# Kernel tuning notes

Measured on AMD Instinct MI355X. Metric: run time of the kernel, lower is better.

The kernel has to match this reference:

```python
import jax, jax.numpy as jnp
import numpy as np

WIN = 9  # window_size (isotropic, module default)
EPS = 1e-5


def _box_sum3d(x, win):
    """Sum over a win^3 box, same-size output ('same' padding). x: [B,1,D,H,W].
    The ones kernel is separable, so apply three 1D convolutions."""
    pad = win // 2
    for ax in range(3):  # spatial axes D,H,W
        kshape = [1, 1, 1, 1, 1]
        kshape[2 + ax] = win
        k = jnp.ones(kshape, x.dtype)
        padding = [(0, 0)] * 3
        padding[ax] = (pad, pad)
        x = jax.lax.conv_general_dilated(x, k, window_strides=(1, 1, 1), padding=padding)
    return x


def setup_inputs() -> dict:
    key = jax.random.key(0)
    k1, k2 = jax.random.split(key)
    shape = (2, 1, 160, 192, 160)
    y_pred = jax.random.normal(k1, shape, dtype=jnp.float32)
    y_true = jax.random.normal(k2, shape, dtype=jnp.float32)
    return {"y_pred": y_pred, "y_true": y_true}


def reference(y_pred, y_true):
    I, J = y_true, y_pred
    win_size = jnp.asarray(WIN ** 3, I.dtype)  # 729

    I_sum = _box_sum3d(I, WIN)
    J_sum = _box_sum3d(J, WIN)
    I2_sum = _box_sum3d(I * I, WIN)
    J2_sum = _box_sum3d(J * J, WIN)
    IJ_sum = _box_sum3d(I * J, WIN)

    I_mean = I_sum / win_size
    J_mean = J_sum / win_size

    cross = IJ_sum - J_mean * I_sum - I_mean * J_sum + I_mean * J_mean * win_size
    I_var = I2_sum - 2 * I_mean * I_sum + I_mean * I_mean * win_size
    J_var = J2_sum - 2 * J_mean * J_sum + J_mean * J_mean * win_size

    cc = cross * cross / (I_var * J_var + EPS)
    return -jnp.mean(cc)
```

## Files before the change

kernel.cpp:

```cpp
#include <hip/hip_runtime.h>
#include <hip/hip_fp16.h>


#define B_    2
#define D_    160
#define H_    192
#define W_    160
#define HW_   (H_*W_)

#define RS    12
#define SLS   (24*RS)
#define FS    (2*SLS)
#define ZROW  (5*FS)
#define ZEND  (ZROW + 16)
#define HSUM0 ZEND
#define HCS   160
#define HRS   10
#define REDU  (HSUM0 + 10*HCS)
#define SMEM  (REDU + 8)
#define DC    40
#define ZCH   (D_/DC)
#define NMAC  ((DC+8)/2)
#define W3I   (1.0f/729.0f)
#define NTOT  9830400.0f

#if __has_builtin(__builtin_amdgcn_rcpf)
#define RCP(x) __builtin_amdgcn_rcpf(x)
#else
#define RCP(x) (1.0f/(x))
#endif

typedef _Float16 half8 __attribute__((ext_vector_type(8)));
typedef float    f32x4 __attribute__((ext_vector_type(4)));
typedef unsigned u32x2 __attribute__((ext_vector_type(2)));
#define MFMA16(a,b,c) __builtin_amdgcn_mfma_f32_16x16x32_f16((a),(b),(c),0,0,0)

#if __has_builtin(__builtin_amdgcn_permlane32_swap)
#define PL32(a,b) do { u32x2 _s = __builtin_amdgcn_permlane32_swap((a),(b),false,false); \
                       (a)=_s[0]; (b)=_s[1]; } while(0)
#else
#define PL32(a,b) asm volatile("s_nop 1\nv_permlane32_swap_b32 %0, %1" : "+v"(a), "+v"(b))
#endif
#if __has_builtin(__builtin_amdgcn_permlane16_swap)
#define PL16(a,b) do { u32x2 _s = __builtin_amdgcn_permlane16_swap((a),(b),false,false); \
                       (a)=_s[0]; (b)=_s[1]; } while(0)
#else
#define PL16(a,b) asm volatile("s_nop 1\nv_permlane16_swap_b32 %0, %1" : "+v"(a), "+v"(b))
#endif

struct __align__(8) HP { __half2 a, b; };

__global__ __launch_bounds__(256, 4) void ncc_fused(const float* __restrict__ gI,
                                                    const float* __restrict__ gJ,
                                                    float* __restrict__ out)
{
  __shared__ __align__(16) float sm[SMEM];
  const int tid  = threadIdx.x;
  const int lane = tid & 63;
  const int Q    = tid >> 6;
  const int n15  = lane & 15;
  const int q4   = lane >> 4;
  const int w0   = blockIdx.x * 16;
  const int h0   = blockIdx.y * 16;
  const int bz   = blockIdx.z;
  const int bb   = bz / ZCH;
  const int d_lo = (bz % ZCH) * DC;

  for (int i = tid; i < ZEND; i += 256) sm[i] = 0.f;

  half8 SEL;
  #pragma unroll
  for (int j = 0; j < 8; ++j) {
    const int k = 8*q4 + j;
    SEL[j] = (k >= n15 && k <= n15 + 8) ? (_Float16)1 : (_Float16)0;
  }

  bool val0 = false, val1 = false;
  int  lo0 = 0, lo1 = 0, sc0 = 0, sc1 = 0;
  const float *pi0 = gI, *pj0 = gJ, *pi1 = gI, *pj1 = gJ;
  {
    auto prep = [&](int t, bool& val, int& lo, int& sc,
                    const float*& pi, const float*& pj) {
      if (t >= 288) { val = false; return; }
      sc = t / 144;
      const int u = t - sc*144;
      const int r = u / 6, c = u - r*6;
      const int gh = h0 - 4 + r, gw = w0 - 4 + 4*c;
      val = ((unsigned)gh < (unsigned)H_) && (gw >= 0) && (gw + 3 < W_);
      lo  = sc*SLS + r*RS + 2*c;
      const long off = ((long)(bb*D_ + (d_lo - 4 + sc))*H_ + gh)*(long)W_ + gw;
      pi = gI + off; pj = gJ + off;
    };
    prep(tid, val0, lo0, sc0, pi0, pj0);
    prep((tid >= 224) ? tid + 32 : 512, val1, lo1, sc1, pi1, pj1);
  }

  int rb_[3], hb_[3];
  #pragma unroll
  for (int i = 0; i < 3; ++i) {
    int c = Q + 4*i; if (c > 9) c = 9;
    rb_[i] = (c % 5)*FS + (c / 5)*SLS;
    hb_[i] = HSUM0 + c*HCS;
  }
  const int a1r = n15*RS + 4*q4;
  const int a2r = (n15 < 8) ? ((16 + n15)*RS + 4*q4) : -1;
  const int zr  = ZROW + 4*q4;

  const int rh = tid >> 4, rw = tid & 15;
  const int rbase = HSUM0 + rw*HRS + (rh >> 1);
  const int rsh   = (rh & 1) * 16;

  float ring[5][9], S[5];
  #pragma unroll
  for (int f = 0; f < 5; ++f) {
    S[f] = 0.f;
    #pragma unroll
    for (int k = 0; k < 9; ++k) ring[f][k] = 0.f;
  }
  float acc = 0.f;

  float4 f0i = {0,0,0,0}, f0j = {0,0,0,0}, f1i = {0,0,0,0}, f1j = {0,0,0,0};
  auto fetch = [&](int sbase) {
    if (val0 && (unsigned)(sbase + sc0) < (unsigned)D_) {
      f0i = *(const float4*)pi0; f0j = *(const float4*)pj0;
    } else { f0i = make_float4(0,0,0,0); f0j = make_float4(0,0,0,0); }
    pi0 += 2*HW_; pj0 += 2*HW_;
    if (val1 && (unsigned)(sbase + sc1) < (unsigned)D_) {
      f1i = *(const float4*)pi1; f1j = *(const float4*)pj1;
    } else { f1i = make_float4(0,0,0,0); f1j = make_float4(0,0,0,0); }
    pi1 += 2*HW_; pj1 += 2*HW_;
  };

  auto stage_one = [&](int lo, float4 fi, float4 fj) {
    const __half2 i01 = __floats2half2_rn(fi.x, fi.y);
    const __half2 i23 = __floats2half2_rn(fi.z, fi.w);
    const __half2 j01 = __floats2half2_rn(fj.x, fj.y);
    const __half2 j23 = __floats2half2_rn(fj.z, fj.w);
    HP hI; hI.a = i01; hI.b = i23;
    HP hJ; hJ.a = j01; hJ.b = j23;
    HP h2; h2.a = __hmul2(i01, i01); h2.b = __hmul2(i23, i23);
    HP h3; h3.a = __hmul2(j01, j01); h3.b = __hmul2(j23, j23);
    HP h4; h4.a = __hmul2(i01, j01); h4.b = __hmul2(i23, j23);
    *(HP*)&sm[lo]        = hI;
    *(HP*)&sm[lo +   FS] = hJ;
    *(HP*)&sm[lo + 2*FS] = h2;
    *(HP*)&sm[lo + 3*FS] = h3;
    *(HP*)&sm[lo + 4*FS] = h4;
  };
  auto stage_write = [&]() {
    if (val0) stage_one(lo0, f0i, f0j);
    if (val1) stage_one(lo1, f1i, f1j);
  };

  auto chain = [&](int rb, int hb) {
    const half8 A1 = *(const half8*)&sm[rb + a1r];
    const half8 A2 = (a2r >= 0) ? *(const half8*)&sm[rb + a2r]
                                : *(const half8*)&sm[zr];
    const f32x4 z = {0.f, 0.f, 0.f, 0.f};
    const f32x4 d1 = MFMA16(A1, SEL, z);
    const f32x4 d2 = MFMA16(A2, SEL, z);
    unsigned t0 = __builtin_bit_cast(unsigned, __floats2half2_rn(d1[0], d1[1]));
    unsigned t1 = __builtin_bit_cast(unsigned, __floats2half2_rn(d1[2], d1[3]));
    unsigned u0 = __builtin_bit_cast(unsigned, __floats2half2_rn(d2[0], d2[1]));
    unsigned u1 = __builtin_bit_cast(unsigned, __floats2half2_rn(d2[2], d2[3]));
    PL32(t0, u0);
    PL32(t1, u1);
    PL16(t0, u0);
    PL16(t1, u1);
    union { unsigned u[4]; half8 h; } Bv;
    Bv.u[0] = t0; Bv.u[1] = t1; Bv.u[2] = u0; Bv.u[3] = u1;
    const f32x4 dh = MFMA16(SEL, Bv.h, z);
    HP ph; ph.a = __floats2half2_rn(dh[0], dh[1]); ph.b = __floats2half2_rn(dh[2], dh[3]);
    *(HP*)&sm[hb + n15*HRS + 2*q4] = ph;
  };

  auto h2ext = [&](int addr) -> float {
    const unsigned u = *(const unsigned*)&sm[addr];
    return __half2float(__ushort_as_half((unsigned short)(u >> rsh)));
  };
  auto ring_cc = [&](int m) {
    float nA[5], nB[5];
    #pragma unroll
    for (int f = 0; f < 5; ++f) {
      nA[f] = h2ext(rbase + f*HCS);
      nB[f] = h2ext(rbase + (5 + f)*HCS);
    }
    float SA[5], SB[5];
    #pragma unroll
    for (int f = 0; f < 5; ++f) {
      SA[f] = S[f]  + nA[f] - ring[f][8];
      SB[f] = SA[f] + nB[f] - ring[f][7];
      S[f]  = SB[f];
      #pragma unroll
      for (int k = 8; k >= 2; --k) ring[f][k] = ring[f][k-2];
      ring[f][1] = nA[f]; ring[f][0] = nB[f];
    }
    if (m >= 4) {
      {
        const float cr = SA[4] - SA[0]*SA[1]*W3I;
        const float vi = SA[2] - SA[0]*SA[0]*W3I;
        const float vj = SA[3] - SA[1]*SA[1]*W3I;
        acc += cr*cr * RCP(vi*vj + 1e-5f);
      }
      {
        const float cr = SB[4] - SB[0]*SB[1]*W3I;
        const float vi = SB[2] - SB[0]*SB[0]*W3I;
        const float vj = SB[3] - SB[1]*SB[1]*W3I;
        acc += cr*cr * RCP(vi*vj + 1e-5f);
      }
    }
  };

  fetch(d_lo - 4);
  __syncthreads();
  stage_write();
  fetch(d_lo - 2);
  __syncthreads();

  for (int m = 0; m < NMAC; ++m) {
    chain(rb_[0], hb_[0]);
    chain(rb_[1], hb_[1]);
    if (Q < 2) chain(rb_[2], hb_[2]);
    __syncthreads();
    if (m + 1 < NMAC) { stage_write(); fetch(d_lo + 2*m); }
    ring_cc(m);
    __syncthreads();
  }

  float v = acc;
  #pragma unroll
  for (int off = 32; off > 0; off >>= 1)
    v += __shfl_down(v, off, 64);
  if (lane == 0) sm[REDU + Q] = v;
  __syncthreads();
  if (tid == 0) {
    const float t = sm[REDU] + sm[REDU+1] + sm[REDU+2] + sm[REDU+3];
    atomicAdd(out, -t / NTOT);
  }
}

extern "C" void kernel_launch(void* const* d_in, const int* in_sizes, int n_in,
                              void* d_out, int out_size, void* d_ws, size_t ws_size,
                              hipStream_t stream) {
  const float* J = (const float*)d_in[0];
  const float* I = (const float*)d_in[1];
  float* outp = (float*)d_out;
  hipMemsetAsync(d_out, 0, sizeof(float), stream);
  dim3 grid(W_/16, H_/16, B_*ZCH);
  ncc_fused<<<grid, dim3(256), 0, stream>>>(I, J, outp);
}
```

Before: 147.4 us.

## Process four depth slices per macro-step instead of two

Each iteration of the main loop now stages four depth slices into shared memory instead of two, and all five field chains run for every slice without the idle-wave imbalance. This halves the number of loop iterations and barriers, and the running box sum advances four slices per step. Each thread now handles three load slots, with the third fetched synchronously inside stage_write, which exposes its latency. Shared memory and register use also grow, which may lower occupancy.

```diff
diff --git a/kernel.cpp b/kernel.cpp
--- a/kernel.cpp
+++ b/kernel.cpp
@@ -10,17 +10,17 @@
 
 #define RS    12
 #define SLS   (24*RS)
-#define FS    (2*SLS)
-#define ZROW  (5*FS)
+#define FS4   (4*SLS)
+#define ZROW  (5*FS4)
 #define ZEND  (ZROW + 16)
 #define HSUM0 ZEND
 #define HCS   160
 #define HRS   10
-#define REDU  (HSUM0 + 10*HCS)
+#define REDU  (HSUM0 + 20*HCS)
 #define SMEM  (REDU + 8)
 #define DC    40
 #define ZCH   (D_/DC)
-#define NMAC  ((DC+8)/2)
+#define NMAC  ((DC+8)/4)
 #define W3I   (1.0f/729.0f)
 #define NTOT  9830400.0f
 
@@ -75,13 +75,13 @@
     SEL[j] = (k >= n15 && k <= n15 + 8) ? (_Float16)1 : (_Float16)0;
   }
 
-  bool val0 = false, val1 = false;
-  int  lo0 = 0, lo1 = 0, sc0 = 0, sc1 = 0;
-  const float *pi0 = gI, *pj0 = gJ, *pi1 = gI, *pj1 = gJ;
+  bool val0 = false, val1 = false, val2 = false;
+  int  lo0 = 0, lo1 = 0, lo2 = 0, sc0 = 0, sc1 = 0, sc2 = 0;
+  const float *pi0 = gI, *pj0 = gJ, *pi1 = gI, *pj1 = gJ, *pi2 = gI, *pj2 = gJ;
   {
     auto prep = [&](int t, bool& val, int& lo, int& sc,
                     const float*& pi, const float*& pj) {
-      if (t >= 288) { val = false; return; }
+      if (t >= 576) { val = false; return; }
       sc = t / 144;
       const int u = t - sc*144;
       const int r = u / 6, c = u - r*6;
@@ -91,16 +91,16 @@
       const long off = ((long)(bb*D_ + (d_lo - 4 + sc))*H_ + gh)*(long)W_ + gw;
       pi = gI + off; pj = gJ + off;
     };
-    prep(tid, val0, lo0, sc0, pi0, pj0);
-    prep((tid >= 224) ? tid + 32 : 512, val1, lo1, sc1, pi1, pj1);
-  }
-
-  int rb_[3], hb_[3];
-  #pragma unroll
-  for (int i = 0; i < 3; ++i) {
-    int c = Q + 4*i; if (c > 9) c = 9;
-    rb_[i] = (c % 5)*FS + (c / 5)*SLS;
-    hb_[i] = HSUM0 + c*HCS;
+    prep(tid,       val0, lo0, sc0, pi0, pj0);
+    prep(tid + 256, val1, lo1, sc1, pi1, pj1);
+    prep((tid < 64) ? tid + 512 : 576, val2, lo2, sc2, pi2, pj2);
+  }
+
+  int rb_[5], hb_[5];
+  #pragma unroll
+  for (int i = 0; i < 5; ++i) {
+    rb_[i] = i*FS4 + Q*SLS;
+    hb_[i] = HSUM0 + (Q*5 + i)*HCS;
   }
   const int a1r = n15*RS + 4*q4;
   const int a2r = (n15 < 8) ? ((16 + n15)*RS + 4*q4) : -1;
@@ -120,15 +120,17 @@
   float acc = 0.f;
 
   float4 f0i = {0,0,0,0}, f0j = {0,0,0,0}, f1i = {0,0,0,0}, f1j = {0,0,0,0};
+  int sb_cur = 0;
   auto fetch = [&](int sbase) {
+    sb_cur = sbase;
     if (val0 && (unsigned)(sbase + sc0) < (unsigned)D_) {
       f0i = *(const float4*)pi0; f0j = *(const float4*)pj0;
     } else { f0i = make_float4(0,0,0,0); f0j = make_float4(0,0,0,0); }
-    pi0 += 2*HW_; pj0 += 2*HW_;
+    pi0 += 4*HW_; pj0 += 4*HW_;
     if (val1 && (unsigned)(sbase + sc1) < (unsigned)D_) {
       f1i = *(const float4*)pi1; f1j = *(const float4*)pj1;
     } else { f1i = make_float4(0,0,0,0); f1j = make_float4(0,0,0,0); }
-    pi1 += 2*HW_; pj1 += 2*HW_;
+    pi1 += 4*HW_; pj1 += 4*HW_;
   };
 
   auto stage_one = [&](int lo, float4 fi, float4 fj) {
@@ -141,15 +143,20 @@
     HP h2; h2.a = __hmul2(i01, i01); h2.b = __hmul2(i23, i23);
     HP h3; h3.a = __hmul2(j01, j01); h3.b = __hmul2(j23, j23);
     HP h4; h4.a = __hmul2(i01, j01); h4.b = __hmul2(i23, j23);
-    *(HP*)&sm[lo]        = hI;
-    *(HP*)&sm[lo +   FS] = hJ;
-    *(HP*)&sm[lo + 2*FS] = h2;
-    *(HP*)&sm[lo + 3*FS] = h3;
-    *(HP*)&sm[lo + 4*FS] = h4;
+    *(HP*)&sm[lo]         = hI;
+    *(HP*)&sm[lo +   FS4] = hJ;
+    *(HP*)&sm[lo + 2*FS4] = h2;
+    *(HP*)&sm[lo + 3*FS4] = h3;
+    *(HP*)&sm[lo + 4*FS4] = h4;
   };
   auto stage_write = [&]() {
+    float4 f2i = {0,0,0,0}, f2j = {0,0,0,0};
+    const bool do2 = val2 && (unsigned)(sb_cur + sc2) < (unsigned)D_;
+    if (do2) { f2i = *(const float4*)pi2; f2j = *(const float4*)pj2; }
+    pi2 += 4*HW_; pj2 += 4*HW_;
     if (val0) stage_one(lo0, f0i, f0j);
     if (val1) stage_one(lo1, f1i, f1j);
+    if (val2) stage_one(lo2, f2i, f2j);
   };
 
   auto chain = [&](int rb, int hb) {
@@ -178,51 +185,47 @@
     const unsigned u = *(const unsigned*)&sm[addr];
     return __half2float(__ushort_as_half((unsigned short)(u >> rsh)));
   };
+  auto cc_eval = [&](const float* Sx) {
+    const float cr = Sx[4] - Sx[0]*Sx[1]*W3I;
+    const float vi = Sx[2] - Sx[0]*Sx[0]*W3I;
+    const float vj = Sx[3] - Sx[1]*Sx[1]*W3I;
+    acc += cr*cr * RCP(vi*vj + 1e-5f);
+  };
   auto ring_cc = [&](int m) {
-    float nA[5], nB[5];
+    float n0[5], n1[5], n2[5], n3[5];
     #pragma unroll
     for (int f = 0; f < 5; ++f) {
-      nA[f] = h2ext(rbase + f*HCS);
-      nB[f] = h2ext(rbase + (5 + f)*HCS);
+      n0[f] = h2ext(rbase + (     f)*HCS);
+      n1[f] = h2ext(rbase + ( 5 + f)*HCS);
+      n2[f] = h2ext(rbase + (10 + f)*HCS);
+      n3[f] = h2ext(rbase + (15 + f)*HCS);
     }
-    float SA[5], SB[5];
+    float SA[5], SB[5], SC[5], SD[5];
     #pragma unroll
     for (int f = 0; f < 5; ++f) {
-      SA[f] = S[f]  + nA[f] - ring[f][8];
-      SB[f] = SA[f] + nB[f] - ring[f][7];
-      S[f]  = SB[f];
-      #pragma unroll
-      for (int k = 8; k >= 2; --k) ring[f][k] = ring[f][k-2];
-      ring[f][1] = nA[f]; ring[f][0] = nB[f];
+      SA[f] = S[f]  + n0[f] - ring[f][8];
+      SB[f] = SA[f] + n1[f] - ring[f][7];
+      SC[f] = SB[f] + n2[f] - ring[f][6];
+      SD[f] = SC[f] + n3[f] - ring[f][5];
+      S[f]  = SD[f];
+      ring[f][8] = ring[f][4]; ring[f][7] = ring[f][3]; ring[f][6] = ring[f][2];
+      ring[f][5] = ring[f][1]; ring[f][4] = ring[f][0];
+      ring[f][3] = n0[f]; ring[f][2] = n1[f]; ring[f][1] = n2[f]; ring[f][0] = n3[f];
     }
-    if (m >= 4) {
-      {
-        const float cr = SA[4] - SA[0]*SA[1]*W3I;
-        const float vi = SA[2] - SA[0]*SA[0]*W3I;
-        const float vj = SA[3] - SA[1]*SA[1]*W3I;
-        acc += cr*cr * RCP(vi*vj + 1e-5f);
-      }
-      {
-        const float cr = SB[4] - SB[0]*SB[1]*W3I;
-        const float vi = SB[2] - SB[0]*SB[0]*W3I;
-        const float vj = SB[3] - SB[1]*SB[1]*W3I;
-        acc += cr*cr * RCP(vi*vj + 1e-5f);
-      }
-    }
+    if (m >= 2) { cc_eval(SA); cc_eval(SB); cc_eval(SC); cc_eval(SD); }
   };
 
   fetch(d_lo - 4);
   __syncthreads();
   stage_write();
-  fetch(d_lo - 2);
+  fetch(d_lo);
   __syncthreads();
 
   for (int m = 0; m < NMAC; ++m) {
-    chain(rb_[0], hb_[0]);
-    chain(rb_[1], hb_[1]);
-    if (Q < 2) chain(rb_[2], hb_[2]);
+    #pragma unroll
+    for (int i = 0; i < 5; ++i) chain(rb_[i], hb_[i]);
     __syncthreads();
-    if (m + 1 < NMAC) { stage_write(); fetch(d_lo + 2*m); }
+    if (m + 1 < NMAC) { stage_write(); fetch(d_lo + 4 + 4*m); }
     ring_cc(m);
     __syncthreads();
   }
```

Result: slower. 153.2 us (+3.9%).

## Double-buffer staging and H-sum LDS buffers, drop one barrier, lengthen depth chunk

Applied to the files above, without the earlier changes.

The raw fp16 staging area and the H-sum LDS area are each split into two buffers that alternate by iteration parity. The next slice is staged while the MFMA chains read the current one, which removes one of the two __syncthreads per depth step. The depth chunk per block is doubled from 40 to 80, so the 8-slice halo is re-read less often. In exchange LDS use per block roughly doubles, and the grid shrinks to 480 blocks, which may leave CUs underused or unevenly loaded.

```diff
diff --git a/kernel.cpp b/kernel.cpp
--- a/kernel.cpp
+++ b/kernel.cpp
@@ -11,14 +11,16 @@
 #define RS    12
 #define SLS   (24*RS)
 #define FS    (2*SLS)
-#define ZROW  (5*FS)
+#define RAWSZ (5*FS)
+#define ZROW  (2*RAWSZ)
 #define ZEND  (ZROW + 16)
 #define HSUM0 ZEND
 #define HCS   160
 #define HRS   10
-#define REDU  (HSUM0 + 10*HCS)
+#define HSZ   (10*HCS)
+#define REDU  (HSUM0 + 2*HSZ)
 #define SMEM  (REDU + 8)
-#define DC    40
+#define DC    80
 #define ZCH   (D_/DC)
 #define NMAC  ((DC+8)/2)
 #define W3I   (1.0f/729.0f)
@@ -147,9 +149,10 @@
     *(HP*)&sm[lo + 3*FS] = h3;
     *(HP*)&sm[lo + 4*FS] = h4;
   };
-  auto stage_write = [&]() {
-    if (val0) stage_one(lo0, f0i, f0j);
-    if (val1) stage_one(lo1, f1i, f1j);
+  auto stage_write = [&](int buf) {
+    const int b = buf * RAWSZ;
+    if (val0) stage_one(b + lo0, f0i, f0j);
+    if (val1) stage_one(b + lo1, f1i, f1j);
   };
 
   auto chain = [&](int rb, int hb) {
@@ -178,12 +181,12 @@
     const unsigned u = *(const unsigned*)&sm[addr];
     return __half2float(__ushort_as_half((unsigned short)(u >> rsh)));
   };
-  auto ring_cc = [&](int m) {
+  auto ring_cc = [&](int m, int hB) {
     float nA[5], nB[5];
     #pragma unroll
     for (int f = 0; f < 5; ++f) {
-      nA[f] = h2ext(rbase + f*HCS);
-      nB[f] = h2ext(rbase + (5 + f)*HCS);
+      nA[f] = h2ext(rbase + hB + f*HCS);
+      nB[f] = h2ext(rbase + hB + (5 + f)*HCS);
     }
     float SA[5], SB[5];
     #pragma unroll
@@ -213,18 +216,19 @@
 
   fetch(d_lo - 4);
   __syncthreads();
-  stage_write();
+  stage_write(0);
   fetch(d_lo - 2);
   __syncthreads();
 
   for (int m = 0; m < NMAC; ++m) {
-    chain(rb_[0], hb_[0]);
-    chain(rb_[1], hb_[1]);
-    if (Q < 2) chain(rb_[2], hb_[2]);
+    const int rB = (m & 1) * RAWSZ;
+    const int hB = (m & 1) * HSZ;
+    chain(rB + rb_[0], hB + hb_[0]);
+    chain(rB + rb_[1], hB + hb_[1]);
+    if (Q < 2) chain(rB + rb_[2], hB + hb_[2]);
+    if (m + 1 < NMAC) { stage_write((m + 1) & 1); fetch(d_lo + 2*m); }
     __syncthreads();
-    if (m + 1 < NMAC) { stage_write(); fetch(d_lo + 2*m); }
-    ring_cc(m);
-    __syncthreads();
+    ring_cc(m, hB);
   }
 
   float v = acc;
```

After: 139.9 us. 5.1% less time.
